# Kernel tuning notes

Hardware: AMD Instinct MI355X
Metric: run time of the kernel (lower is better)

The kernel has to match this reference:

```python
import jax, jax.numpy as jnp
import numpy as np

OUT_DIM = 4096
IN_DIM = 4096
N_NNZ = 1600000
BATCH = 8192


def setup_inputs() -> dict:
    key = jax.random.key(0)
    k1, k2, k3 = jax.random.split(key, 3)
    x = jax.random.normal(k1, (BATCH, IN_DIM), dtype=jnp.float32)
    # COO indices of the transposed kernel: (row=output idx, col=input idx)
    rows = jax.random.randint(k2, (N_NNZ, 1), 0, OUT_DIM, dtype=jnp.int64)
    cols = jax.random.randint(jax.random.fold_in(k2, 1), (N_NNZ, 1), 0, IN_DIM, dtype=jnp.int64)
    indices = jnp.concatenate([rows, cols], axis=1)  # (N_NNZ, 2)
    values = jax.random.normal(k3, (N_NNZ,), dtype=jnp.float32) * 0.02
    return {"x": x, "indices": indices, "values": values}


def reference(x, indices, values):
    # kernel_t is a sparse (OUT_DIM, IN_DIM) matrix. In JAX the efficient
    # faithful form is to scatter the nonzeros into a dense matrix (duplicate
    # indices sum, matching SpMM semantics) and do a single dense GEMM.
    rows = indices[:, 0]
    cols = indices[:, 1]
    W_t = jnp.zeros((OUT_DIM, IN_DIM), dtype=values.dtype).at[rows, cols].add(values)
    # output = (kernel_t @ x^T)^T = x @ kernel_t^T, then ReLU activation.
    out = jax.nn.relu(jnp.einsum("bi,oi->bo", x, W_t))
    return out
```

## Files before the change

kernel.cpp:

```cpp
#include <hip/hip_runtime.h>
#include <hip/hip_bf16.h>
#include <stdint.h>

#define M_DIM 8192
#define N_DIM 4096
#define K_DIM 4096
#define NNZ   1600000

typedef __attribute__((ext_vector_type(8))) short bf16x8;
typedef __attribute__((ext_vector_type(4))) float f32x4;

static const size_t WF32_OFF  = 0;
static const size_t WBF16_OFF = 64ull << 20;
static const size_t XB_OFF    = 96ull << 20;
static const size_t WS_NEED   = 160ull << 20;

__device__ __forceinline__ unsigned short f2bf(float f) {
    union { float f; uint32_t u; } a; a.f = f;
    uint32_t u = a.u;
    uint32_t r = (u + 0x7FFFu + ((u >> 16) & 1u)) >> 16;
    return (unsigned short)r;
}

__global__ void scatter_kernel(const int* __restrict__ idx,
                               const float* __restrict__ vals,
                               float* __restrict__ W) {
    int t = blockIdx.x * blockDim.x + threadIdx.x;
    if (t < NNZ) {
        int2 rc = ((const int2*)idx)[t];
        atomicAdd(&W[(size_t)rc.x * K_DIM + rc.y], vals[t]);
    }
}

__global__ void convert_both_kernel(const float* __restrict__ W,
                                    const float* __restrict__ x,
                                    unsigned short* __restrict__ Wb,
                                    unsigned short* __restrict__ xb,
                                    int n4W, int n4T) {
    int t = blockIdx.x * blockDim.x + threadIdx.x;
    if (t >= n4T) return;
    const float* src; unsigned short* dst; int i;
    if (t < n4W) { src = W; dst = Wb; i = t; }
    else         { src = x; dst = xb; i = t - n4W; }
    float4 v = ((const float4*)src)[i];
    ushort4 o;
    o.x = f2bf(v.x); o.y = f2bf(v.y); o.z = f2bf(v.z); o.w = f2bf(v.w);
    ((ushort4*)dst)[i] = o;
}

#define GLOAD16(gp, lp) __builtin_amdgcn_global_load_lds( \
    (const __attribute__((address_space(1))) void*)(gp),  \
    (__attribute__((address_space(3))) void*)(lp), 16, 0, 0)
#define VMCNT(n)   asm volatile("s_waitcnt vmcnt(" #n ")" ::: "memory")
#define BAR()    __builtin_amdgcn_s_barrier()

#define FRAG(T, r, kk) \
    (*(const bf16x8*)&(T)[(r) * 64 + (((((kk) << 2) + l4) ^ ((r) & 7)) << 3)])

#define STAGE_AG(buf, tt, g) \
    GLOAD16(Ab + (size_t)((g) * 64 + rbase) * K_DIM + (size_t)(tt) * 64 + cs, \
            &sA[buf][(g) * 4096 + wid * 512])
#define STAGE_BG(buf, tt, g) \
    GLOAD16(Bb + (size_t)((g) * 64 + rbase) * K_DIM + (size_t)(tt) * 64 + cs, \
            &sB[buf][(g) * 4096 + wid * 512])

__global__ __launch_bounds__(512, 2) void gemm256_v8(
        const __hip_bfloat16* __restrict__ A,
        const __hip_bfloat16* __restrict__ B,
        float* __restrict__ C)
{
    __shared__ __align__(16) __hip_bfloat16 sA[2][256 * 64];
    __shared__ __align__(16) __hip_bfloat16 sB[2][256 * 64];

    const int tid  = threadIdx.x;
    const int lane = tid & 63;
    const int wid  = tid >> 6;
    const int wr   = wid >> 2;
    const int wc   = wid & 3;
    const int l15  = lane & 15, l4 = lane >> 4;

    const int bid = blockIdx.x;
    const int swz = (bid & 7) * 64 + (bid >> 3);
    const int m0  = (swz >> 4) * 256;
    const int n0  = (swz & 15) * 256;

    const int rbase = tid >> 3;
    const int cs    = ((tid & 7) ^ (rbase & 7)) << 3;

    const __hip_bfloat16* Ab = A + (size_t)m0 * K_DIM;
    const __hip_bfloat16* Bb = B + (size_t)n0 * K_DIM;

    f32x4 acc[8][4] = {};

    STAGE_AG(0, 0, 0); STAGE_AG(0, 0, 1); STAGE_AG(0, 0, 2); STAGE_AG(0, 0, 3);
    STAGE_BG(0, 0, 0); STAGE_BG(0, 0, 1); STAGE_BG(0, 0, 2); STAGE_BG(0, 0, 3);
    STAGE_AG(1, 1, 0); STAGE_AG(1, 1, 1); STAGE_AG(1, 1, 2); STAGE_AG(1, 1, 3);
    STAGE_BG(1, 1, 0); STAGE_BG(1, 1, 1);
    VMCNT(6);
    BAR();

    const int NT = K_DIM / 64;
    #pragma unroll 2
    for (int t = 0; t < NT; ++t) {
        const int c = t & 1;
        const __hip_bfloat16* TA = sA[c];
        const __hip_bfloat16* TB = sB[c];

        bf16x8 aLo[4][2], aHi[4][2], bLo[2][2], bHi[2][2];

        #pragma unroll
        for (int m = 0; m < 4; ++m) {
            const int r = wr * 128 + m * 16 + l15;
            aLo[m][0] = FRAG(TA, r, 0);
            aLo[m][1] = FRAG(TA, r, 1);
        }
        #pragma unroll
        for (int n = 0; n < 2; ++n) {
            const int r = wc * 64 + n * 16 + l15;
            bLo[n][0] = FRAG(TB, r, 0);
            bLo[n][1] = FRAG(TB, r, 1);
        }
        __builtin_amdgcn_s_setprio(1);
        #pragma unroll
        for (int k = 0; k < 2; ++k)
            #pragma unroll
            for (int m = 0; m < 4; ++m)
                #pragma unroll
                for (int n = 0; n < 2; ++n)
                    acc[m][n] = __builtin_amdgcn_mfma_f32_16x16x32_bf16(
                                    aLo[m][k], bLo[n][k], acc[m][n], 0, 0, 0);
        __builtin_amdgcn_s_setprio(0);
        if (t + 1 < NT) { STAGE_BG(c ^ 1, t + 1, 2); STAGE_BG(c ^ 1, t + 1, 3); }
        #pragma unroll
        for (int m = 0; m < 4; ++m) {
            const int r = wr * 128 + 64 + m * 16 + l15;
            aHi[m][0] = FRAG(TA, r, 0);
            aHi[m][1] = FRAG(TA, r, 1);
        }
        BAR();

        if (t + 2 < NT) {
            STAGE_AG(c, t + 2, 0); STAGE_AG(c, t + 2, 1);
            STAGE_AG(c, t + 2, 2); STAGE_AG(c, t + 2, 3);
        }
        __builtin_amdgcn_s_setprio(1);
        #pragma unroll
        for (int k = 0; k < 2; ++k)
            #pragma unroll
            for (int m = 0; m < 4; ++m)
                #pragma unroll
                for (int n = 0; n < 2; ++n)
                    acc[4 + m][n] = __builtin_amdgcn_mfma_f32_16x16x32_bf16(
                                    aHi[m][k], bLo[n][k], acc[4 + m][n], 0, 0, 0);
        __builtin_amdgcn_s_setprio(0);
        #pragma unroll
        for (int n = 0; n < 2; ++n) {
            const int r = wc * 64 + 32 + n * 16 + l15;
            bHi[n][0] = FRAG(TB, r, 0);
            bHi[n][1] = FRAG(TB, r, 1);
        }
        BAR();

        if (t + 2 < NT) { STAGE_BG(c, t + 2, 0); STAGE_BG(c, t + 2, 1); }
        __builtin_amdgcn_s_setprio(1);
        #pragma unroll
        for (int k = 0; k < 2; ++k)
            #pragma unroll
            for (int m = 0; m < 4; ++m)
                #pragma unroll
                for (int n = 0; n < 2; ++n)
                    acc[4 + m][2 + n] = __builtin_amdgcn_mfma_f32_16x16x32_bf16(
                                    aHi[m][k], bHi[n][k], acc[4 + m][2 + n], 0, 0, 0);
        #pragma unroll
        for (int k = 0; k < 2; ++k)
            #pragma unroll
            for (int m = 0; m < 4; ++m)
                #pragma unroll
                for (int n = 0; n < 2; ++n)
                    acc[m][2 + n] = __builtin_amdgcn_mfma_f32_16x16x32_bf16(
                                    aLo[m][k], bHi[n][k], acc[m][2 + n], 0, 0, 0);
        __builtin_amdgcn_s_setprio(0);

        if (t < NT - 2) {
            VMCNT(6);
            BAR();
        } else if (t == NT - 2) {
            VMCNT(0);
            BAR();
        }
    }

    const int row_base = m0 + wr * 128;
    const int col_base = n0 + wc * 64;
    #pragma unroll
    for (int m = 0; m < 8; ++m)
        #pragma unroll
        for (int n = 0; n < 4; ++n) {
            const f32x4 v = acc[m][n];
            const int col = col_base + n * 16 + l15;
            #pragma unroll
            for (int j = 0; j < 4; ++j) {
                const int row = row_base + m * 16 + l4 * 4 + j;
                C[(size_t)row * N_DIM + col] = fmaxf(v[j], 0.0f);
            }
        }
}

__global__ void gemm_f32_fallback(const float* __restrict__ A,
                                  const float* __restrict__ W,
                                  float* __restrict__ C) {
    __shared__ float As[64][17];
    __shared__ float Bs[64][17];
    const int tx = threadIdx.x & 15, ty = threadIdx.x >> 4;
    const int m0 = blockIdx.y * 64, n0 = blockIdx.x * 64;
    float acc[4][4] = {};
    for (int kt = 0; kt < K_DIM; kt += 16) {
        #pragma unroll
        for (int i = 0; i < 4; ++i) {
            int e = threadIdx.x + i * 256;
            int r = e >> 4, k = e & 15;
            As[r][k] = A[(size_t)(m0 + r) * K_DIM + kt + k];
            Bs[r][k] = W[(size_t)(n0 + r) * K_DIM + kt + k];
        }
        __syncthreads();
        #pragma unroll
        for (int k = 0; k < 16; ++k) {
            float av[4], bv[4];
            #pragma unroll
            for (int i = 0; i < 4; ++i) av[i] = As[ty * 4 + i][k];
            #pragma unroll
            for (int i = 0; i < 4; ++i) bv[i] = Bs[tx * 4 + i][k];
            #pragma unroll
            for (int i = 0; i < 4; ++i)
                #pragma unroll
                for (int j = 0; j < 4; ++j) acc[i][j] += av[i] * bv[j];
        }
        __syncthreads();
    }
    #pragma unroll
    for (int i = 0; i < 4; ++i)
        #pragma unroll
        for (int j = 0; j < 4; ++j)
            C[(size_t)(m0 + ty * 4 + i) * N_DIM + n0 + tx * 4 + j] =
                fmaxf(acc[i][j], 0.0f);
}

extern "C" void kernel_launch(void* const* d_in, const int* in_sizes, int n_in,
                              void* d_out, int out_size, void* d_ws, size_t ws_size,
                              hipStream_t stream) {
    const float* x       = (const float*)d_in[0];
    const int*   indices = (const int*)d_in[1];
    const float* values  = (const float*)d_in[2];
    float*       out     = (float*)d_out;

    float* Wf = (float*)((char*)d_ws + WF32_OFF);

    hipMemsetAsync(Wf, 0, (size_t)N_DIM * K_DIM * sizeof(float), stream);
    scatter_kernel<<<(NNZ + 255) / 256, 256, 0, stream>>>(indices, values, Wf);

    if (ws_size >= WS_NEED) {
        unsigned short* Wb = (unsigned short*)((char*)d_ws + WBF16_OFF);
        unsigned short* xb = (unsigned short*)((char*)d_ws + XB_OFF);

        const int n4W = (N_DIM * K_DIM) / 4;
        const int n4T = n4W + (M_DIM * K_DIM) / 4;
        convert_both_kernel<<<(n4T + 255) / 256, 256, 0, stream>>>(
            Wf, x, Wb, xb, n4W, n4T);

        gemm256_v8<<<(M_DIM / 256) * (N_DIM / 256), 512, 0, stream>>>(
            (const __hip_bfloat16*)xb, (const __hip_bfloat16*)Wb, out);
    } else {
        gemm_f32_fallback<<<dim3(N_DIM / 64, M_DIM / 64), 256, 0, stream>>>(
            x, Wf, out);
    }
}
```

Measured before the change: 363.2 us.

## Restructure GEMM main loop into k-half register pipeline with full-tile prefetch

Replaces the quadrant-based schedule in the 256x256 bf16 MFMA GEMM with a two-phase k-split. The k=0 fragments for the full 8x4 tile are preloaded into registers, and the k=1 fragments are read while the k=0 MFMAs run. The next tile's k=0 fragments are loaded after a full vmcnt(0) wait, and all A/B staging for tile t+2 is issued at once after a barrier. This aims to cut barriers and interleave LDS reads with MFMA work. It holds more fragment registers live and waits for all outstanding global loads each iteration, which may reduce latency hiding and occupancy.

After: 1.085 ms. 2.99x slower.

```diff
diff --git a/kernel.cpp b/kernel.cpp
--- a/kernel.cpp
+++ b/kernel.cpp
@@ -64,7 +64,7 @@
     GLOAD16(Bb + (size_t)((g) * 64 + rbase) * K_DIM + (size_t)(tt) * 64 + cs, \
             &sB[buf][(g) * 4096 + wid * 512])
 
-__global__ __launch_bounds__(512, 2) void gemm256_v8(
+__global__ __launch_bounds__(512, 2) void gemm256_v10(
         const __hip_bfloat16* __restrict__ A,
         const __hip_bfloat16* __restrict__ B,
         float* __restrict__ C)
@@ -91,13 +91,18 @@
     const __hip_bfloat16* Bb = B + (size_t)n0 * K_DIM;
 
     f32x4 acc[8][4] = {};
+    bf16x8 a0[8], b0[4], a1[8], b1[4];
 
     STAGE_AG(0, 0, 0); STAGE_AG(0, 0, 1); STAGE_AG(0, 0, 2); STAGE_AG(0, 0, 3);
     STAGE_BG(0, 0, 0); STAGE_BG(0, 0, 1); STAGE_BG(0, 0, 2); STAGE_BG(0, 0, 3);
     STAGE_AG(1, 1, 0); STAGE_AG(1, 1, 1); STAGE_AG(1, 1, 2); STAGE_AG(1, 1, 3);
-    STAGE_BG(1, 1, 0); STAGE_BG(1, 1, 1);
-    VMCNT(6);
+    STAGE_BG(1, 1, 0); STAGE_BG(1, 1, 1); STAGE_BG(1, 1, 2); STAGE_BG(1, 1, 3);
+    VMCNT(8);
     BAR();
+    #pragma unroll
+    for (int m = 0; m < 8; ++m) a0[m] = FRAG(sA[0], wr * 128 + m * 16 + l15, 0);
+    #pragma unroll
+    for (int n = 0; n < 4; ++n) b0[n] = FRAG(sB[0], wc * 64 + n * 16 + l15, 0);
 
     const int NT = K_DIM / 64;
     #pragma unroll 2
@@ -106,87 +111,48 @@
         const __hip_bfloat16* TA = sA[c];
         const __hip_bfloat16* TB = sB[c];
 
-        bf16x8 aLo[4][2], aHi[4][2], bLo[2][2], bHi[2][2];
-
-        #pragma unroll
-        for (int m = 0; m < 4; ++m) {
-            const int r = wr * 128 + m * 16 + l15;
-            aLo[m][0] = FRAG(TA, r, 0);
-            aLo[m][1] = FRAG(TA, r, 1);
-        }
-        #pragma unroll
-        for (int n = 0; n < 2; ++n) {
-            const int r = wc * 64 + n * 16 + l15;
-            bLo[n][0] = FRAG(TB, r, 0);
-            bLo[n][1] = FRAG(TB, r, 1);
-        }
+        #pragma unroll
+        for (int m = 0; m < 8; ++m) a1[m] = FRAG(TA, wr * 128 + m * 16 + l15, 1);
+        #pragma unroll
+        for (int n = 0; n < 4; ++n) b1[n] = FRAG(TB, wc * 64 + n * 16 + l15, 1);
+
         __builtin_amdgcn_s_setprio(1);
         #pragma unroll
-        for (int k = 0; k < 2; ++k)
-            #pragma unroll
-            for (int m = 0; m < 4; ++m)
-                #pragma unroll
-                for (int n = 0; n < 2; ++n)
-                    acc[m][n] = __builtin_amdgcn_mfma_f32_16x16x32_bf16(
-                                    aLo[m][k], bLo[n][k], acc[m][n], 0, 0, 0);
+        for (int m = 0; m < 8; ++m)
+            #pragma unroll
+            for (int n = 0; n < 4; ++n)
+                acc[m][n] = __builtin_amdgcn_mfma_f32_16x16x32_bf16(
+                                a0[m], b0[n], acc[m][n], 0, 0, 0);
         __builtin_amdgcn_s_setprio(0);
-        if (t + 1 < NT) { STAGE_BG(c ^ 1, t + 1, 2); STAGE_BG(c ^ 1, t + 1, 3); }
-        #pragma unroll
-        for (int m = 0; m < 4; ++m) {
-            const int r = wr * 128 + 64 + m * 16 + l15;
-            aHi[m][0] = FRAG(TA, r, 0);
-            aHi[m][1] = FRAG(TA, r, 1);
-        }
-        BAR();
-
-        if (t + 2 < NT) {
-            STAGE_AG(c, t + 2, 0); STAGE_AG(c, t + 2, 1);
-            STAGE_AG(c, t + 2, 2); STAGE_AG(c, t + 2, 3);
-        }
-        __builtin_amdgcn_s_setprio(1);
-        #pragma unroll
-        for (int k = 0; k < 2; ++k)
-            #pragma unroll
-            for (int m = 0; m < 4; ++m)
-                #pragma unroll
-                for (int n = 0; n < 2; ++n)
-                    acc[4 + m][n] = __builtin_amdgcn_mfma_f32_16x16x32_bf16(
-                                    aHi[m][k], bLo[n][k], acc[4 + m][n], 0, 0, 0);
-        __builtin_amdgcn_s_setprio(0);
-        #pragma unroll
-        for (int n = 0; n < 2; ++n) {
-            const int r = wc * 64 + 32 + n * 16 + l15;
-            bHi[n][0] = FRAG(TB, r, 0);
-            bHi[n][1] = FRAG(TB, r, 1);
-        }
-        BAR();
-
-        if (t + 2 < NT) { STAGE_BG(c, t + 2, 0); STAGE_BG(c, t + 2, 1); }
-        __builtin_amdgcn_s_setprio(1);
-        #pragma unroll
-        for (int k = 0; k < 2; ++k)
-            #pragma unroll
-            for (int m = 0; m < 4; ++m)
-                #pragma unroll
-                for (int n = 0; n < 2; ++n)
-                    acc[4 + m][2 + n] = __builtin_amdgcn_mfma_f32_16x16x32_bf16(
-                                    aHi[m][k], bHi[n][k], acc[4 + m][2 + n], 0, 0, 0);
-        #pragma unroll
-        for (int k = 0; k < 2; ++k)
-            #pragma unroll
-            for (int m = 0; m < 4; ++m)
-                #pragma unroll
-                for (int n = 0; n < 2; ++n)
-                    acc[m][2 + n] = __builtin_amdgcn_mfma_f32_16x16x32_bf16(
-                                    aLo[m][k], bHi[n][k], acc[m][2 + n], 0, 0, 0);
-        __builtin_amdgcn_s_setprio(0);
-
-        if (t < NT - 2) {
-            VMCNT(6);
-            BAR();
-        } else if (t == NT - 2) {
+
+        if (t + 1 < NT) {
             VMCNT(0);
             BAR();
+            const __hip_bfloat16* TAn = sA[c ^ 1];
+            const __hip_bfloat16* TBn = sB[c ^ 1];
+            #pragma unroll
+            for (int m = 0; m < 8; ++m) a0[m] = FRAG(TAn, wr * 128 + m * 16 + l15, 0);
+            #pragma unroll
+            for (int n = 0; n < 4; ++n) b0[n] = FRAG(TBn, wc * 64 + n * 16 + l15, 0);
+        }
+
+        __builtin_amdgcn_s_setprio(1);
+        #pragma unroll
+        for (int m = 0; m < 8; ++m)
+            #pragma unroll
+            for (int n = 0; n < 4; ++n)
+                acc[m][n] = __builtin_amdgcn_mfma_f32_16x16x32_bf16(
+                                a1[m], b1[n], acc[m][n], 0, 0, 0);
+        __builtin_amdgcn_s_setprio(0);
+
+        if (t + 1 < NT) {
+            BAR();
+            if (t + 2 < NT) {
+                STAGE_AG(c, t + 2, 0); STAGE_AG(c, t + 2, 1);
+                STAGE_AG(c, t + 2, 2); STAGE_AG(c, t + 2, 3);
+                STAGE_BG(c, t + 2, 0); STAGE_BG(c, t + 2, 1);
+                STAGE_BG(c, t + 2, 2); STAGE_BG(c, t + 2, 3);
+            }
         }
     }
 
@@ -267,7 +233,7 @@
         convert_both_kernel<<<(n4T + 255) / 256, 256, 0, stream>>>(
             Wf, x, Wb, xb, n4W, n4T);
 
-        gemm256_v8<<<(M_DIM / 256) * (N_DIM / 256), 512, 0, stream>>>(
+        gemm256_v10<<<(M_DIM / 256) * (N_DIM / 256), 512, 0, stream>>>(
             (const __hip_bfloat16*)xb, (const __hip_bfloat16*)Wb, out);
     } else {
         gemm_f32_fallback<<<dim3(N_DIM / 64, M_DIM / 64), 256, 0, stream>>>(
```
